# Kernel tuning notes

Hardware: AMD Instinct MI355X
Metric: run time of the kernel (lower is better)

The kernel has to match this reference:

```python
import jax, jax.numpy as jnp
import numpy as np

EPS = 1e-8
SCALES = (1, 3, 5, 7)


def _depthwise_conv1d(x_bcl, w, k):
    # x_bcl: [B, C, L], w: [C, 1, k] (torch depthwise layout = OIH with groups=C)
    C = x_bcl.shape[1]
    return jax.lax.conv_general_dilated(
        x_bcl, w, window_strides=(1,), padding=[(k // 2, k // 2)],
        dimension_numbers=("NCH", "OIH", "NCH"), feature_group_count=C)


def _channel_rmsnorm(h_bcl, scale):
    # RMSNorm over channel dim of [B, C, L]
    rms = jnp.sqrt(jnp.mean(h_bcl * h_bcl, axis=1, keepdims=True))
    return scale[None, :, None] * h_bcl / (rms + EPS)


def setup_inputs() -> dict:
    key = jax.random.key(0)
    B, L, C, D = 16, 4096, 256, 512
    ns = len(SCALES)
    Dp = D // ns          # 128 per-scale channels
    Dh = D // 4           # 128 attention hidden
    ks = jax.random.split(key, 16)
    inp = {"x": jax.random.normal(ks[0], (B, L, C), dtype=jnp.float32)}
    for i, k in enumerate(SCALES):
        inp[f"dw{k}"] = jax.random.normal(ks[1 + i], (C, 1, k), dtype=jnp.float32) * 0.1
        inp[f"pw{k}"] = jax.random.normal(ks[5 + i], (Dp, C), dtype=jnp.float32) * 0.05
        inp[f"cn{k}"] = jnp.ones((Dp,), dtype=jnp.float32)
    inp["attn_w1"] = jax.random.normal(ks[9], (Dh, D), dtype=jnp.float32) * 0.05
    inp["attn_b1"] = jnp.zeros((Dh,), dtype=jnp.float32)
    inp["attn_w2"] = jax.random.normal(ks[10], (ns, Dh), dtype=jnp.float32) * 0.05
    inp["attn_b2"] = jnp.zeros((ns,), dtype=jnp.float32)
    inp["final_w"] = jax.random.normal(ks[11], (D, D), dtype=jnp.float32) * 0.04
    inp["norm_scale"] = jnp.ones((D,), dtype=jnp.float32)
    inp["res_w"] = jax.random.normal(ks[12], (D, C), dtype=jnp.float32) * 0.05
    return inp


def reference(x, dw1, dw3, dw5, dw7, pw1, pw3, pw5, pw7, cn1, cn3, cn5, cn7,
              attn_w1, attn_b1, attn_w2, attn_b2, final_w, norm_scale, res_w):
    dws = {1: dw1, 3: dw3, 5: dw5, 7: dw7}
    pws = {1: pw1, 3: pw3, 5: pw5, 7: pw7}
    cns = {1: cn1, 3: cn3, 5: cn5, 7: cn7}

    residual = jnp.einsum("blc,dc->bld", x, res_w)  # Linear(input_dim->latent_dim)
    x_t = jnp.transpose(x, (0, 2, 1))               # [B, C, L]

    feats = []
    for k in SCALES:
        h = _depthwise_conv1d(x_t, dws[k], k)                # [B, C, L]
        h = jnp.einsum("bcl,oc->bol", h, pws[k])             # 1x1 conv -> [B, Dp, L]
        h = _channel_rmsnorm(h, cns[k])
        feats.append(jax.nn.gelu(h, approximate=False))

    multi_scale = jnp.concatenate(feats, axis=1)             # [B, D, L]
    a = jnp.einsum("bcl,oc->bol", multi_scale, attn_w1) + attn_b1[None, :, None]
    a = jax.nn.gelu(a, approximate=False)
    a = jnp.einsum("bcl,oc->bol", a, attn_w2) + attn_b2[None, :, None]
    attn = jax.nn.softmax(a, axis=1)                         # [B, num_scales, L]

    weighted = [f * attn[:, i:i + 1, :] for i, f in enumerate(feats)]
    combined = jnp.concatenate(weighted, axis=1)             # [B, D, L]
    out = jnp.einsum("bcl,oc->blo", combined, final_w)       # final 1x1 conv + transpose
    out = out + residual                                     # [B, L, D]

    rms = jnp.sqrt(jnp.mean(out * out, axis=-1, keepdims=True))
    return norm_scale * out / (rms + EPS)
```

## Files before the change

kernel.cpp:

```cpp
#include <hip/hip_runtime.h>
#include <hip/hip_bf16.h>
#include <math.h>

typedef unsigned int u32;
typedef unsigned short u16;

typedef __bf16 bf16_t;
typedef bf16_t bf16x8 __attribute__((ext_vector_type(8)));
typedef float f32x4 __attribute__((ext_vector_type(4)));

#define EPSF 1e-8f

__device__ __forceinline__ float bf2f(u16 h) {
    union { u32 u; float f; } v; v.u = ((u32)h) << 16; return v.f;
}
__device__ __forceinline__ u16 f2bf(float f) {
    union { float ff; u32 u; } v; v.ff = f;
    u32 u = v.u;
    return (u16)((u + 0x7fffu + ((u >> 16) & 1u)) >> 16);
}
__device__ __forceinline__ float gelu_exact(float v) {
    float z = v * 0.70710678118654752440f;
    float az = fabsf(z);
    float t = __builtin_amdgcn_rcpf(__builtin_fmaf(0.3275911f, az, 1.0f));
    float p = __builtin_fmaf(1.061405429f, t, -1.453152027f);
    p = __builtin_fmaf(p, t, 1.421413741f);
    p = __builtin_fmaf(p, t, -0.284496736f);
    p = __builtin_fmaf(p, t, 0.254829592f);
    float e = __expf(-az * az);
    float erfa = 1.0f - p * t * e;
    float er = __builtin_copysignf(erfa, z);
    return 0.5f * v * (1.0f + er);
}
__device__ __forceinline__ void gld_lds16(const void* g, void* l) {
    __builtin_amdgcn_global_load_lds(
        (const __attribute__((address_space(1))) unsigned int*)g,
        (__attribute__((address_space(3))) unsigned int*)l, 16, 0, 0);
}

template<int S>
__device__ __forceinline__ void conv_scale16(
    const float* __restrict__ dw, const float* xc, u16* __restrict__ H, int c)
{
    const int K = 2 * S + 1;
    float d[K];
    #pragma unroll
    for (int j = 0; j < K; j++) d[j] = dw[c * K + j];
    const int chunk = c & ~63;
    const int q6 = (c >> 3) & 7;
    const int jj = c & 7;
    #pragma unroll
    for (int l = 0; l < 16; l++) {
        float a = 0.f;
        #pragma unroll
        for (int j = 0; j < K; j++) a += xc[l + 3 - S + j] * d[j];
        H[(S * 16 + l) * 256 + chunk + ((q6 ^ (l & 7)) << 3) + jj] = f2bf(a);
    }
}

__global__ __launch_bounds__(256) void k_feats(
    const float* __restrict__ x,
    const float* __restrict__ dw1, const float* __restrict__ dw3,
    const float* __restrict__ dw5, const float* __restrict__ dw7,
    const float* __restrict__ cn1, const float* __restrict__ cn3,
    const float* __restrict__ cn5, const float* __restrict__ cn7,
    const u16* __restrict__ pwb, const u16* __restrict__ w1b,
    const float* __restrict__ b1, const float* __restrict__ w2,
    const float* __restrict__ b2,
    u32* __restrict__ feats32)
{
    __shared__ __align__(16) u16 H[4 * 16 * 256];
    float (*part)[16][4] = (float (*)[16][4])(void*)(H + 8320);
    float (*att4)[4]     = (float (*)[4])(void*)(H + 8832);
    const int t = threadIdx.x;
    const int lane = t & 63;
    const int wave = t >> 6;
    const int c15 = lane & 15;
    const int q = lane >> 4;
    const int l0 = blockIdx.x * 16;
    const int b = blockIdx.y;
    const float* xb = x + (size_t)b * 4096 * 256;

    float xc[22];
    #pragma unroll
    for (int r = 0; r < 22; r++) {
        int g = l0 - 3 + r;
        xc[r] = (g >= 0 && g < 4096) ? xb[(size_t)g * 256 + t] : 0.0f;
    }
    conv_scale16<0>(dw1, xc, H, t);
    conv_scale16<1>(dw3, xc, H, t);
    conv_scale16<2>(dw5, xc, H, t);
    conv_scale16<3>(dw7, xc, H, t);
    __syncthreads();

    const int s = wave;
    const u16* wBf = pwb + (size_t)s * 32768;
    f32x4 acc[8];
    #pragma unroll
    for (int nt = 0; nt < 8; nt++) acc[nt] = f32x4{0.f, 0.f, 0.f, 0.f};

    const int row_base = (s * 16 + c15) * 256;
    const int m7 = c15 & 7;
    #pragma unroll 2
    for (int kt = 0; kt < 8; kt++) {
        const int g7 = (((kt & 1) << 2) | q) ^ m7;
        bf16x8 af = *(const bf16x8*)&H[row_base + ((kt >> 1) << 6) + (g7 << 3)];
        #pragma unroll
        for (int nt = 0; nt < 8; nt++) {
            bf16x8 bv = *(const bf16x8*)&wBf[(kt * 8 + nt) * 512 + lane * 8];
            acc[nt] = __builtin_amdgcn_mfma_f32_16x16x32_bf16(af, bv, acc[nt], 0, 0, 0);
        }
    }

    float rinv_[4];
    #pragma unroll
    for (int r = 0; r < 4; r++) {
        float ss = 0.f;
        #pragma unroll
        for (int nt = 0; nt < 8; nt++) ss += acc[nt][r] * acc[nt][r];
        ss += __shfl_xor(ss, 1);
        ss += __shfl_xor(ss, 2);
        ss += __shfl_xor(ss, 4);
        ss += __shfl_xor(ss, 8);
        rinv_[r] = 1.0f / (sqrtf(ss * (1.0f / 128.0f)) + EPSF);
    }

    const float* cn = (s == 0) ? cn1 : (s == 1) ? cn3 : (s == 2) ? cn5 : cn7;
    float cnv[8];
    #pragma unroll
    for (int nt = 0; nt < 8; nt++) cnv[nt] = cn[nt * 16 + c15];

    __syncthreads();

    u16* F = H;
    #pragma unroll
    for (int nt = 0; nt < 8; nt++)
        #pragma unroll
        for (int r = 0; r < 4; r++) {
            const int m = q * 4 + r;
            float g = gelu_exact(acc[nt][r] * rinv_[r] * cnv[nt]);
            F[m * 520 + s * 128 + nt * 16 + c15] = f2bf(g);
        }
    __syncthreads();

    f32x4 a1[2];
    a1[0] = f32x4{0.f, 0.f, 0.f, 0.f};
    a1[1] = f32x4{0.f, 0.f, 0.f, 0.f};
    #pragma unroll 4
    for (int kt = 0; kt < 16; kt++) {
        bf16x8 av = *(const bf16x8*)&F[c15 * 520 + kt * 32 + q * 8];
        bf16x8 bv0 = *(const bf16x8*)&w1b[(kt * 8 + wave * 2) * 512 + lane * 8];
        bf16x8 bv1 = *(const bf16x8*)&w1b[(kt * 8 + wave * 2 + 1) * 512 + lane * 8];
        a1[0] = __builtin_amdgcn_mfma_f32_16x16x32_bf16(av, bv0, a1[0], 0, 0, 0);
        a1[1] = __builtin_amdgcn_mfma_f32_16x16x32_bf16(av, bv1, a1[1], 0, 0, 0);
    }
    {
        const float b1v0 = b1[wave * 32 + c15];
        const float b1v1 = b1[wave * 32 + 16 + c15];
        #pragma unroll
        for (int r = 0; r < 4; r++) {
            a1[0][r] = gelu_exact(a1[0][r] + b1v0);
            a1[1][r] = gelu_exact(a1[1][r] + b1v1);
        }
    }

    float w2v[4][2];
    #pragma unroll
    for (int sc = 0; sc < 4; sc++) {
        w2v[sc][0] = w2[sc * 128 + wave * 32 + c15];
        w2v[sc][1] = w2[sc * 128 + wave * 32 + 16 + c15];
    }
    #pragma unroll
    for (int r = 0; r < 4; r++) {
        float g0 = a1[0][r], g1 = a1[1][r];
        float p0 = g0 * w2v[0][0] + g1 * w2v[0][1];
        float p1 = g0 * w2v[1][0] + g1 * w2v[1][1];
        float p2 = g0 * w2v[2][0] + g1 * w2v[2][1];
        float p3 = g0 * w2v[3][0] + g1 * w2v[3][1];
        #pragma unroll
        for (int msk = 1; msk < 16; msk <<= 1) {
            p0 += __shfl_xor(p0, msk);
            p1 += __shfl_xor(p1, msk);
            p2 += __shfl_xor(p2, msk);
            p3 += __shfl_xor(p3, msk);
        }
        if (c15 == 0) {
            const int m = q * 4 + r;
            part[wave][m][0] = p0; part[wave][m][1] = p1;
            part[wave][m][2] = p2; part[wave][m][3] = p3;
        }
    }
    __syncthreads();

    if (t < 64) {
        const int m = t >> 2, sc = t & 3;
        float tot = part[0][m][sc] + part[1][m][sc] + part[2][m][sc] + part[3][m][sc] + b2[sc];
        float mx = fmaxf(tot, __shfl_xor(tot, 1));
        mx = fmaxf(mx, __shfl_xor(mx, 2));
        float e = __expf(tot - mx);
        float sum = e + __shfl_xor(e, 1);
        sum += __shfl_xor(sum, 2);
        att4[m][sc] = e * __builtin_amdgcn_rcpf(sum);
    }
    __syncthreads();

    const size_t row0 = (size_t)b * 4096 + l0;
    #pragma unroll
    for (int it = 0; it < 4; it++) {
        const int r4 = it * 4 + wave;
        const float a = att4[r4][lane >> 4];
        uint4 v = *(const uint4*)&F[r4 * 520 + lane * 8];
        u32 o0 = (u32)f2bf(bf2f((u16)(v.x & 0xffffu)) * a) | ((u32)f2bf(bf2f((u16)(v.x >> 16)) * a) << 16);
        u32 o1 = (u32)f2bf(bf2f((u16)(v.y & 0xffffu)) * a) | ((u32)f2bf(bf2f((u16)(v.y >> 16)) * a) << 16);
        u32 o2 = (u32)f2bf(bf2f((u16)(v.z & 0xffffu)) * a) | ((u32)f2bf(bf2f((u16)(v.z >> 16)) * a) << 16);
        u32 o3 = (u32)f2bf(bf2f((u16)(v.w & 0xffffu)) * a) | ((u32)f2bf(bf2f((u16)(v.w >> 16)) * a) << 16);
        *(uint4*)&feats32[(row0 + r4) * 256 + lane * 4] = make_uint4(o0, o1, o2, o3);
    }
}

__global__ __launch_bounds__(256) void k_packw(
    const float* __restrict__ fw, const float* __restrict__ rw, u16* __restrict__ wbf)
{
    const int n = blockIdx.x;
    const int k = blockIdx.y * 256 + threadIdx.x;
    float v = (k < 512) ? fw[(size_t)n * 512 + k] : rw[(size_t)n * 256 + (k - 512)];
    const int kt = k >> 5, q = (k >> 3) & 3, j = k & 7;
    const int nw = n >> 7, ni = (n >> 4) & 7, c15 = n & 15;
    wbf[(size_t)(kt * 32 + nw * 8 + ni) * 512 + q * 128 + c15 * 8 + j] = f2bf(v);
}

__global__ __launch_bounds__(256) void k_packpw(
    const float* __restrict__ pw1, const float* __restrict__ pw3,
    const float* __restrict__ pw5, const float* __restrict__ pw7,
    u16* __restrict__ pwb)
{
    const int s = blockIdx.y;
    const float* pw = (s == 0) ? pw1 : (s == 1) ? pw3 : (s == 2) ? pw5 : pw7;
    const int i = blockIdx.x * 256 + threadIdx.x;
    const int o = i >> 8, c = i & 255;
    const int dst = ((c >> 5) * 8 + (o >> 4)) * 512 + ((c >> 3) & 3) * 128 + (o & 15) * 8 + (c & 7);
    pwb[(size_t)s * 32768 + dst] = f2bf(pw[i]);
}

__global__ __launch_bounds__(256) void k_packw1(
    const float* __restrict__ w1, u16* __restrict__ w1b)
{
    const int i = blockIdx.x * 256 + threadIdx.x;
    const int o = i >> 9, c = i & 511;
    const int dst = ((c >> 5) * 8 + (o >> 4)) * 512 + ((c >> 3) & 3) * 128 + (o & 15) * 8 + (c & 7);
    w1b[dst] = f2bf(w1[i]);
}

__global__ __launch_bounds__(512, 2) void k_final_norm(
    const u16* __restrict__ feats, const float* __restrict__ x,
    const u16* __restrict__ wbf, const float* __restrict__ nsc,
    float* __restrict__ out)
{
    __shared__ __align__(16) u16 Fa[64 * 512];
    __shared__ __align__(16) u16 Xa[64 * 256];
    __shared__ float part[2][32][4];
    const int t = threadIdx.x;
    const int lane = t & 63;
    const int wave = t >> 6;
    const int c15 = lane & 15;
    const int q = lane >> 4;
    const int mw = wave >> 2;
    const int nw = wave & 3;
    const int m0 = blockIdx.x * 64;

    #pragma unroll
    for (int i = 0; i < 8; i++) {
        const int r = i * 8 + wave;
        gld_lds16(feats + (size_t)(m0 + r) * 512 + (size_t)((lane ^ (r & 15)) * 8),
                  &Fa[r * 512]);
    }
    {
        const int r = t >> 3, sub = t & 7;
        const float4* xp = (const float4*)(x + (size_t)(m0 + r) * 256 + sub * 32);
        #pragma unroll
        for (int uu = 0; uu < 4; uu++) {
            float4 v0 = xp[2 * uu], v1 = xp[2 * uu + 1];
            u32 p0 = (u32)f2bf(v0.x) | ((u32)f2bf(v0.y) << 16);
            u32 p1 = (u32)f2bf(v0.z) | ((u32)f2bf(v0.w) << 16);
            u32 p2 = (u32)f2bf(v1.x) | ((u32)f2bf(v1.y) << 16);
            u32 p3 = (u32)f2bf(v1.z) | ((u32)f2bf(v1.w) << 16);
            const int u = (sub * 4 + uu) ^ (r & 15);
            *(uint4*)&Xa[r * 256 + u * 8] = make_uint4(p0, p1, p2, p3);
        }
    }
    __syncthreads();

    f32x4 acc[2][8];
    #pragma unroll
    for (int i = 0; i < 2; i++)
        #pragma unroll
        for (int j = 0; j < 8; j++) acc[i][j] = f32x4{0.f, 0.f, 0.f, 0.f};

    const int ra0 = mw * 32 + c15;
    const int ra1 = mw * 32 + 16 + c15;

    #pragma unroll 2
    for (int kt = 0; kt < 16; ++kt) {
        bf16x8 af0 = *(const bf16x8*)&Fa[ra0 * 512 + (((kt * 4 + q) ^ (ra0 & 15)) * 8)];
        bf16x8 af1 = *(const bf16x8*)&Fa[ra1 * 512 + (((kt * 4 + q) ^ (ra1 & 15)) * 8)];
        #pragma unroll
        for (int ni = 0; ni < 8; ni++) {
            bf16x8 bv = *(const bf16x8*)&wbf[(size_t)(kt * 32 + nw * 8 + ni) * 512 + lane * 8];
            acc[0][ni] = __builtin_amdgcn_mfma_f32_16x16x32_bf16(af0, bv, acc[0][ni], 0, 0, 0);
            acc[1][ni] = __builtin_amdgcn_mfma_f32_16x16x32_bf16(af1, bv, acc[1][ni], 0, 0, 0);
        }
    }
    #pragma unroll 2
    for (int kt = 16; kt < 24; ++kt) {
        const int v2 = (kt - 16) * 4 + q;
        bf16x8 af0 = *(const bf16x8*)&Xa[ra0 * 256 + ((v2 ^ (ra0 & 15)) * 8)];
        bf16x8 af1 = *(const bf16x8*)&Xa[ra1 * 256 + ((v2 ^ (ra1 & 15)) * 8)];
        #pragma unroll
        for (int ni = 0; ni < 8; ni++) {
            bf16x8 bv = *(const bf16x8*)&wbf[(size_t)(kt * 32 + nw * 8 + ni) * 512 + lane * 8];
            acc[0][ni] = __builtin_amdgcn_mfma_f32_16x16x32_bf16(af0, bv, acc[0][ni], 0, 0, 0);
            acc[1][ni] = __builtin_amdgcn_mfma_f32_16x16x32_bf16(af1, bv, acc[1][ni], 0, 0, 0);
        }
    }

    #pragma unroll
    for (int mt = 0; mt < 2; mt++)
        #pragma unroll
        for (int r = 0; r < 4; r++) {
            float ss = 0.f;
            #pragma unroll
            for (int ni = 0; ni < 8; ni++) ss += acc[mt][ni][r] * acc[mt][ni][r];
            ss += __shfl_xor(ss, 1);
            ss += __shfl_xor(ss, 2);
            ss += __shfl_xor(ss, 4);
            ss += __shfl_xor(ss, 8);
            if (c15 == 0) part[mw][mt * 16 + q * 4 + r][nw] = ss;
        }
    __syncthreads();

    float nscv[8];
    #pragma unroll
    for (int ni = 0; ni < 8; ni++) nscv[ni] = nsc[nw * 128 + ni * 16 + c15];

    #pragma unroll
    for (int mt = 0; mt < 2; mt++) {
        #pragma unroll
        for (int r = 0; r < 4; r++) {
            const int row = mt * 16 + q * 4 + r;
            float tot = part[mw][row][0] + part[mw][row][1]
                      + part[mw][row][2] + part[mw][row][3];
            float rv = 1.0f / (sqrtf(tot * (1.0f / 512.0f)) + EPSF);
            float* orow = out + (size_t)(m0 + mw * 32 + row) * 512 + nw * 128 + c15;
            #pragma unroll
            for (int ni = 0; ni < 8; ni++)
                orow[ni * 16] = acc[mt][ni][r] * rv * nscv[ni];
        }
    }
}

extern "C" void kernel_launch(void* const* d_in, const int* in_sizes, int n_in,
                              void* d_out, int out_size, void* d_ws, size_t ws_size,
                              hipStream_t stream)
{
    const float* x   = (const float*)d_in[0];
    const float* dw1 = (const float*)d_in[1];
    const float* pw1 = (const float*)d_in[2];
    const float* cn1 = (const float*)d_in[3];
    const float* dw3 = (const float*)d_in[4];
    const float* pw3 = (const float*)d_in[5];
    const float* cn3 = (const float*)d_in[6];
    const float* dw5 = (const float*)d_in[7];
    const float* pw5 = (const float*)d_in[8];
    const float* cn5 = (const float*)d_in[9];
    const float* dw7 = (const float*)d_in[10];
    const float* pw7 = (const float*)d_in[11];
    const float* cn7 = (const float*)d_in[12];
    const float* w1  = (const float*)d_in[13];
    const float* b1  = (const float*)d_in[14];
    const float* w2  = (const float*)d_in[15];
    const float* b2  = (const float*)d_in[16];
    const float* fw  = (const float*)d_in[17];
    const float* nsc = (const float*)d_in[18];
    const float* rw  = (const float*)d_in[19];

    u16* feats = (u16*)d_ws;
    u16* wbf   = (u16*)((char*)d_ws + (size_t)67108864);
    u16* pwb   = (u16*)((char*)d_ws + (size_t)67895296);
    u16* w1b   = (u16*)d_out;
    float* out = (float*)d_out;
    if (ws_size < (size_t)68157440) return;

    k_packw<<<dim3(512, 3), 256, 0, stream>>>(fw, rw, wbf);
    k_packpw<<<dim3(128, 4), 256, 0, stream>>>(pw1, pw3, pw5, pw7, pwb);
    k_packw1<<<dim3(256), 256, 0, stream>>>(w1, w1b);
    k_feats<<<dim3(256, 16), 256, 0, stream>>>(x, dw1, dw3, dw5, dw7,
                                               cn1, cn3, cn5, cn7, pwb, w1b,
                                               b1, w2, b2, (u32*)feats);
    k_final_norm<<<dim3(1024), 512, 0, stream>>>(feats, x, wbf, nsc, out);
}
```

Before: 432.9 us.

## Merge weight-pack kernels and retile final GEMM with double-buffered B loads

Folds the three weight-packing kernels into one launch to cut launch overhead. The final GEMM+RMSNorm kernel moves from 64-row, 8-wave blocks to 32-row, 4-wave blocks. The grid grows to 2048 blocks and LDS per block shrinks, which should allow more resident blocks. B-fragment global loads are double-buffered in registers so the next k-step's weights load while the current MFMAs run. The trade-off is that each block reuses its weight loads across fewer rows, which raises global/L2 weight traffic, and the extra buffers raise register pressure.

```diff
diff --git a/kernel.cpp b/kernel.cpp
--- a/kernel.cpp
+++ b/kernel.cpp
@@ -218,59 +218,54 @@
     }
 }
 
-__global__ __launch_bounds__(256) void k_packw(
-    const float* __restrict__ fw, const float* __restrict__ rw, u16* __restrict__ wbf)
-{
-    const int n = blockIdx.x;
-    const int k = blockIdx.y * 256 + threadIdx.x;
-    float v = (k < 512) ? fw[(size_t)n * 512 + k] : rw[(size_t)n * 256 + (k - 512)];
-    const int kt = k >> 5, q = (k >> 3) & 3, j = k & 7;
-    const int nw = n >> 7, ni = (n >> 4) & 7, c15 = n & 15;
-    wbf[(size_t)(kt * 32 + nw * 8 + ni) * 512 + q * 128 + c15 * 8 + j] = f2bf(v);
-}
-
-__global__ __launch_bounds__(256) void k_packpw(
+__global__ __launch_bounds__(256) void k_pack(
+    const float* __restrict__ fw, const float* __restrict__ rw,
     const float* __restrict__ pw1, const float* __restrict__ pw3,
     const float* __restrict__ pw5, const float* __restrict__ pw7,
-    u16* __restrict__ pwb)
+    const float* __restrict__ w1,
+    u16* __restrict__ wbf, u16* __restrict__ pwb, u16* __restrict__ w1b)
 {
-    const int s = blockIdx.y;
-    const float* pw = (s == 0) ? pw1 : (s == 1) ? pw3 : (s == 2) ? pw5 : pw7;
-    const int i = blockIdx.x * 256 + threadIdx.x;
-    const int o = i >> 8, c = i & 255;
-    const int dst = ((c >> 5) * 8 + (o >> 4)) * 512 + ((c >> 3) & 3) * 128 + (o & 15) * 8 + (c & 7);
-    pwb[(size_t)s * 32768 + dst] = f2bf(pw[i]);
-}
-
-__global__ __launch_bounds__(256) void k_packw1(
-    const float* __restrict__ w1, u16* __restrict__ w1b)
-{
-    const int i = blockIdx.x * 256 + threadIdx.x;
-    const int o = i >> 9, c = i & 511;
-    const int dst = ((c >> 5) * 8 + (o >> 4)) * 512 + ((c >> 3) & 3) * 128 + (o & 15) * 8 + (c & 7);
-    w1b[dst] = f2bf(w1[i]);
-}
-
-__global__ __launch_bounds__(512, 2) void k_final_norm(
+    const u32 idx = blockIdx.x * 256 + threadIdx.x;
+    if (idx < 393216u) {
+        const int n = idx / 768, k = idx - n * 768;
+        float v = (k < 512) ? fw[(size_t)n * 512 + k] : rw[(size_t)n * 256 + (k - 512)];
+        const int kt = k >> 5, q = (k >> 3) & 3, j = k & 7;
+        const int nw = n >> 7, ni = (n >> 4) & 7, c15 = n & 15;
+        wbf[(size_t)(kt * 32 + nw * 8 + ni) * 512 + q * 128 + c15 * 8 + j] = f2bf(v);
+    } else if (idx < 524288u) {
+        const u32 i2 = idx - 393216u;
+        const int s = i2 >> 15;
+        const int i = i2 & 32767;
+        const float* pw = (s == 0) ? pw1 : (s == 1) ? pw3 : (s == 2) ? pw5 : pw7;
+        const int o = i >> 8, c = i & 255;
+        const int dst = ((c >> 5) * 8 + (o >> 4)) * 512 + ((c >> 3) & 3) * 128 + (o & 15) * 8 + (c & 7);
+        pwb[(size_t)s * 32768 + dst] = f2bf(pw[i]);
+    } else {
+        const u32 i = idx - 524288u;
+        const int o = i >> 9, c = i & 511;
+        const int dst = ((c >> 5) * 8 + (o >> 4)) * 512 + ((c >> 3) & 3) * 128 + (o & 15) * 8 + (c & 7);
+        w1b[dst] = f2bf(w1[i]);
+    }
+}
+
+__global__ __launch_bounds__(256) void k_final_norm(
     const u16* __restrict__ feats, const float* __restrict__ x,
     const u16* __restrict__ wbf, const float* __restrict__ nsc,
     float* __restrict__ out)
 {
-    __shared__ __align__(16) u16 Fa[64 * 512];
-    __shared__ __align__(16) u16 Xa[64 * 256];
-    __shared__ float part[2][32][4];
+    __shared__ __align__(16) u16 Fa[32 * 512];
+    __shared__ __align__(16) u16 Xa[32 * 256];
+    __shared__ float part[32][4];
     const int t = threadIdx.x;
     const int lane = t & 63;
     const int wave = t >> 6;
     const int c15 = lane & 15;
     const int q = lane >> 4;
-    const int mw = wave >> 2;
-    const int nw = wave & 3;
-    const int m0 = blockIdx.x * 64;
+    const int m0 = blockIdx.x * 32;
 
     #pragma unroll
     for (int i = 0; i < 8; i++) {
-        const int r = i * 8 + wave;
+        const int r = i * 4 + wave;
         gld_lds16(feats + (size_t)(m0 + r) * 512 + (size_t)((lane ^ (r & 15)) * 8),
                   &Fa[r * 512]);
     }
@@ -296,32 +291,48 @@
         #pragma unroll
         for (int j = 0; j < 8; j++) acc[i][j] = f32x4{0.f, 0.f, 0.f, 0.f};
 
-    const int ra0 = mw * 32 + c15;
-    const int ra1 = mw * 32 + 16 + c15;
-
-    #pragma unroll 2
-    for (int kt = 0; kt < 16; ++kt) {
-        bf16x8 af0 = *(const bf16x8*)&Fa[ra0 * 512 + (((kt * 4 + q) ^ (ra0 & 15)) * 8)];
-        bf16x8 af1 = *(const bf16x8*)&Fa[ra1 * 512 + (((kt * 4 + q) ^ (ra1 & 15)) * 8)];
-        #pragma unroll
-        for (int ni = 0; ni < 8; ni++) {
-            bf16x8 bv = *(const bf16x8*)&wbf[(size_t)(kt * 32 + nw * 8 + ni) * 512 + lane * 8];
-            acc[0][ni] = __builtin_amdgcn_mfma_f32_16x16x32_bf16(af0, bv, acc[0][ni], 0, 0, 0);
-            acc[1][ni] = __builtin_amdgcn_mfma_f32_16x16x32_bf16(af1, bv, acc[1][ni], 0, 0, 0);
-        }
-    }
-    #pragma unroll 2
-    for (int kt = 16; kt < 24; ++kt) {
-        const int v2 = (kt - 16) * 4 + q;
-        bf16x8 af0 = *(const bf16x8*)&Xa[ra0 * 256 + ((v2 ^ (ra0 & 15)) * 8)];
-        bf16x8 af1 = *(const bf16x8*)&Xa[ra1 * 256 + ((v2 ^ (ra1 & 15)) * 8)];
-        #pragma unroll
-        for (int ni = 0; ni < 8; ni++) {
-            bf16x8 bv = *(const bf16x8*)&wbf[(size_t)(kt * 32 + nw * 8 + ni) * 512 + lane * 8];
-            acc[0][ni] = __builtin_amdgcn_mfma_f32_16x16x32_bf16(af0, bv, acc[0][ni], 0, 0, 0);
-            acc[1][ni] = __builtin_amdgcn_mfma_f32_16x16x32_bf16(af1, bv, acc[1][ni], 0, 0, 0);
-        }
-    }
+    const int ra0 = c15;
+    const int ra1 = 16 + c15;
+    const u16* wp = wbf + (size_t)(wave * 8) * 512 + (size_t)lane * 8;
+
+#define LOAD_B(dst, kt)                                                        \
+    _Pragma("unroll")                                                          \
+    for (int ni = 0; ni < 8; ni++)                                             \
+        dst[ni] = *(const bf16x8*)(wp + ((size_t)(kt) * 32 + ni) * 512);
+
+#define COMPUTE(kt, bv)                                                        \
+    {                                                                          \
+        bf16x8 af0, af1;                                                       \
+        if ((kt) < 16) {                                                       \
+            const int u = ((kt) * 4 + q) ^ c15;                                \
+            af0 = *(const bf16x8*)&Fa[ra0 * 512 + u * 8];                      \
+            af1 = *(const bf16x8*)&Fa[ra1 * 512 + u * 8];                      \
+        } else {                                                               \
+            const int u = (((kt) - 16) * 4 + q) ^ c15;                         \
+            af0 = *(const bf16x8*)&Xa[ra0 * 256 + u * 8];                      \
+            af1 = *(const bf16x8*)&Xa[ra1 * 256 + u * 8];                      \
+        }                                                                      \
+        _Pragma("unroll")                                                      \
+        for (int ni = 0; ni < 8; ni++) {                                       \
+            acc[0][ni] = __builtin_amdgcn_mfma_f32_16x16x32_bf16(              \
+                af0, bv[ni], acc[0][ni], 0, 0, 0);                             \
+            acc[1][ni] = __builtin_amdgcn_mfma_f32_16x16x32_bf16(              \
+                af1, bv[ni], acc[1][ni], 0, 0, 0);                             \
+        }                                                                      \
+    }
+
+    bf16x8 bvA[8], bvB[8];
+    LOAD_B(bvA, 0);
+    #pragma unroll
+    for (int kt2 = 0; kt2 < 12; kt2++) {
+        const int k0 = kt2 * 2;
+        LOAD_B(bvB, k0 + 1);
+        COMPUTE(k0, bvA);
+        if (kt2 < 11) { LOAD_B(bvA, k0 + 2); }
+        COMPUTE(k0 + 1, bvB);
+    }
+#undef LOAD_B
+#undef COMPUTE
 
     #pragma unroll
     for (int mt = 0; mt < 2; mt++)
@@ -334,23 +345,22 @@
             ss += __shfl_xor(ss, 2);
             ss += __shfl_xor(ss, 4);
             ss += __shfl_xor(ss, 8);
-            if (c15 == 0) part[mw][mt * 16 + q * 4 + r][nw] = ss;
+            if (c15 == 0) part[mt * 16 + q * 4 + r][wave] = ss;
         }
     __syncthreads();
 
     float nscv[8];
     #pragma unroll
-    for (int ni = 0; ni < 8; ni++) nscv[ni] = nsc[nw * 128 + ni * 16 + c15];
+    for (int ni = 0; ni < 8; ni++) nscv[ni] = nsc[wave * 128 + ni * 16 + c15];
 
     #pragma unroll
     for (int mt = 0; mt < 2; mt++) {
         #pragma unroll
         for (int r = 0; r < 4; r++) {
             const int row = mt * 16 + q * 4 + r;
-            float tot = part[mw][row][0] + part[mw][row][1]
-                      + part[mw][row][2] + part[mw][row][3];
+            float tot = part[row][0] + part[row][1] + part[row][2] + part[row][3];
             float rv = 1.0f / (sqrtf(tot * (1.0f / 512.0f)) + EPSF);
-            float* orow = out + (size_t)(m0 + mw * 32 + row) * 512 + nw * 128 + c15;
+            float* orow = out + (size_t)(m0 + row) * 512 + wave * 128 + c15;
             #pragma unroll
             for (int ni = 0; ni < 8; ni++)
                 orow[ni * 16] = acc[mt][ni][r] * rv * nscv[ni];
@@ -390,11 +400,10 @@
     float* out = (float*)d_out;
     if (ws_size < (size_t)68157440) return;
 
-    k_packw<<<dim3(512, 3), 256, 0, stream>>>(fw, rw, wbf);
-    k_packpw<<<dim3(128, 4), 256, 0, stream>>>(pw1, pw3, pw5, pw7, pwb);
-    k_packw1<<<dim3(256), 256, 0, stream>>>(w1, w1b);
+    k_pack<<<dim3(2304), 256, 0, stream>>>(fw, rw, pw1, pw3, pw5, pw7, w1,
+                                           wbf, pwb, w1b);
     k_feats<<<dim3(256, 16), 256, 0, stream>>>(x, dw1, dw3, dw5, dw7,
                                                cn1, cn3, cn5, cn7, pwb, w1b,
                                                b1, w2, b2, (u32*)feats);
-    k_final_norm<<<dim3(1024), 512, 0, stream>>>(feats, x, wbf, nsc, out);
-}
+    k_final_norm<<<dim3(2048), 256, 0, stream>>>(feats, x, wbf, nsc, out);
+}
```

Result: faster. 410.4 us (-5.2%).
